# Optimization experiments

Measured on AMD Instinct MI355X. Metric: run time of the kernel, lower is better.

Reference implementation:

```python
import jax, jax.numpy as jnp
import numpy as np

TEMPERATURE = 0.5
EPS = 1e-12  # matches torch F.normalize default eps


def _l2_normalize(x):
    norm = jnp.sqrt(jnp.sum(x * x, axis=-1, keepdims=True))
    return x / jnp.maximum(norm, EPS)


def setup_inputs() -> dict:
    key = jax.random.key(0)
    k1, k2 = jax.random.split(key)
    B, C, D = 64, 512, 256
    visual_features = jax.random.normal(k1, (B, C, D), dtype=jnp.float32)
    text_embeddings = jax.random.normal(k2, (B, C, D), dtype=jnp.float32)
    return {"visual_features": visual_features, "text_embeddings": text_embeddings}


def reference(visual_features, text_embeddings):
    v = _l2_normalize(visual_features)   # (B, C, D)
    t = _l2_normalize(text_embeddings)   # (B, C, D)
    # positive: diagonal similarity per class
    sim_pos = jnp.einsum('bcd,bcd->bc', v, t)
    positive = jnp.exp(sim_pos / TEMPERATURE)            # (B, C)
    # full BxCxC similarity matrix
    all_sim = jnp.exp(jnp.einsum('bcd,bkd->bck', v, t) / TEMPERATURE)
    negative = jnp.sum(all_sim, axis=-1) - positive      # (B, C)
    loss = -jnp.log(positive / (positive + negative))
    return jnp.mean(loss)
```

## Files before the change

### kernel.cpp

```cpp
#include <hip/hip_runtime.h>
#include <hip/hip_bf16.h>

#define BB 64
#define CC 512
#define DD 256

typedef __attribute__((ext_vector_type(8))) short bf16x8;
typedef __attribute__((ext_vector_type(4))) float f32x4;
typedef unsigned int u32;

#define SWZ(r) (((r) & 7) << 4)

__device__ inline short f2bf(float f) {
    union { __hip_bfloat16 h; short s; } cv;
    cv.h = __float2bfloat16(f);
    return cv.s;
}

__global__ __launch_bounds__(256) void norm_rows(const float* __restrict__ in,
                                                 unsigned short* __restrict__ out) {
    const int row  = blockIdx.x * 4 + (threadIdx.x >> 6);
    const int lane = threadIdx.x & 63;
    const float4 x = reinterpret_cast<const float4*>(in)[(size_t)row * 64 + lane];
    float ss = x.x * x.x + x.y * x.y + x.z * x.z + x.w * x.w;
#pragma unroll
    for (int off = 32; off; off >>= 1) ss += __shfl_xor(ss, off);
    const float r = 1.0f / fmaxf(sqrtf(ss), 1e-12f);
    ushort4 o;
    o.x = (unsigned short)f2bf(x.x * r);
    o.y = (unsigned short)f2bf(x.y * r);
    o.z = (unsigned short)f2bf(x.z * r);
    o.w = (unsigned short)f2bf(x.w * r);
    reinterpret_cast<ushort4*>(out)[(size_t)row * 64 + lane] = o;
}

__global__ __launch_bounds__(256, 2) void gemm_loss(const float* __restrict__ V,
                                                    const unsigned short* __restrict__ Tn,
                                                    float* __restrict__ partials) {
    __shared__ char lds[65536];

    const int i0 = blockIdx.x;
    const int b  = (i0 & 7) * 8 + ((i0 >> 3) & 7);
    const int rb = i0 >> 6;

    const int tid  = threadIdx.x;
    const int lane = tid & 63;
    const int wave = tid >> 6;
    const int g    = lane >> 4;
    const int ln   = lane & 15;

    const float* gV = V + (size_t)b * (CC * DD) + (size_t)rb * 64 * DD;
    const char*  gT = reinterpret_cast<const char*>(Tn + (size_t)b * (CC * DD));

#pragma unroll
    for (int r2 = 0; r2 < 8; ++r2) {
        const int L   = wave * 8192 + r2 * 1024 + (lane << 4);
        const int row = L >> 9, inrow = L & 511;
        __builtin_amdgcn_global_load_lds((const u32*)(gT + row * 512 + (inrow ^ SWZ(row))),
                                         (u32*)(lds + wave * 8192 + r2 * 1024), 16, 0, 0);
    }

    {
        const int rrow  = tid >> 3;
        const int ecolB = (tid & 7) * 64;
        char* bufA = lds + 32768;
#pragma unroll
        for (int p = 0; p < 2; ++p) {
            const float4* src =
                reinterpret_cast<const float4*>(gV + (size_t)(p * 32 + rrow) * DD) + (tid & 7) * 8;
            float4 x[8];
#pragma unroll
            for (int q = 0; q < 8; ++q) x[q] = src[q];
            float ss = 0.f;
#pragma unroll
            for (int q = 0; q < 8; ++q)
                ss += x[q].x * x[q].x + x[q].y * x[q].y + x[q].z * x[q].z + x[q].w * x[q].w;
            ss += __shfl_xor(ss, 1);
            ss += __shfl_xor(ss, 2);
            ss += __shfl_xor(ss, 4);
            const float rinv = 1.0f / fmaxf(sqrtf(ss), 1e-12f);
            const int row = p * 32 + rrow;
            char* dstrow  = bufA + row * 512;
            const int sw  = SWZ(row);
#pragma unroll
            for (int q2 = 0; q2 < 4; ++q2) {
                const float4 v0 = x[2 * q2], v1 = x[2 * q2 + 1];
                bf16x8 o;
                o[0] = f2bf(v0.x * rinv); o[1] = f2bf(v0.y * rinv);
                o[2] = f2bf(v0.z * rinv); o[3] = f2bf(v0.w * rinv);
                o[4] = f2bf(v1.x * rinv); o[5] = f2bf(v1.y * rinv);
                o[6] = f2bf(v1.z * rinv); o[7] = f2bf(v1.w * rinv);
                *reinterpret_cast<bf16x8*>(dstrow + ((ecolB + q2 * 16) ^ sw)) = o;
            }
        }
    }
    __syncthreads();

    bf16x8 a[4][8];
#pragma unroll
    for (int i = 0; i < 4; ++i) {
        const int row  = i * 16 + ln;
        const char* rp = lds + 32768 + row * 512;
        const int sw   = SWZ(row);
#pragma unroll
        for (int kk = 0; kk < 8; ++kk)
            a[i][kk] = *reinterpret_cast<const bf16x8*>(rp + ((kk * 64 + g * 16) ^ sw));
    }
    __syncthreads();

    float rs[4][4];
    float dg[4][4];
#pragma unroll
    for (int i = 0; i < 4; ++i)
#pragma unroll
        for (int r = 0; r < 4; ++r) { rs[i][r] = 0.f; dg[i][r] = 0.f; }

    for (int ct = 0; ct < 8; ++ct) {
        if (ct < 7) {
            const char* gtile = gT + (size_t)(ct + 1) * 64 * 512;
            char* dst = lds + ((ct & 1) ? 0 : 32768);
#pragma unroll
            for (int r2 = 0; r2 < 8; ++r2) {
                const int L   = wave * 8192 + r2 * 1024 + (lane << 4);
                const int row = L >> 9, inrow = L & 511;
                __builtin_amdgcn_global_load_lds(
                    (const u32*)(gtile + row * 512 + (inrow ^ SWZ(row))),
                    (u32*)(dst + wave * 8192 + r2 * 1024), 16, 0, 0);
            }
        }

        const char* Bc = lds + ((ct & 1) ? 32768 : 0);
        f32x4 acc[4];
#pragma unroll
        for (int i = 0; i < 4; ++i) acc[i] = (f32x4){0.f, 0.f, 0.f, 0.f};
        {
            const int row  = wave * 16 + ln;
            const char* rp = Bc + row * 512;
            const int sw   = SWZ(row);
#pragma unroll
            for (int kk = 0; kk < 8; ++kk) {
                const bf16x8 bb = *reinterpret_cast<const bf16x8*>(rp + ((kk * 64 + g * 16) ^ sw));
#pragma unroll
                for (int i = 0; i < 4; ++i)
                    acc[i] = __builtin_amdgcn_mfma_f32_16x16x32_bf16(a[i][kk], bb, acc[i], 0, 0, 0);
            }
        }

        const int gcol = ct * 64 + wave * 16 + ln;
#pragma unroll
        for (int i = 0; i < 4; ++i) {
            const int grow = rb * 64 + i * 16 + g * 4;
#pragma unroll
            for (int r = 0; r < 4; ++r) {
                const float s2 = acc[i][r] * 2.0f;
                rs[i][r] += __expf(s2);
                if (gcol == grow + r) dg[i][r] += s2;
            }
        }
        __syncthreads();
    }

    float* vred = reinterpret_cast<float*>(lds);
    float* dred = vred + 256;
#pragma unroll
    for (int i = 0; i < 4; ++i)
#pragma unroll
        for (int r = 0; r < 4; ++r) {
            float v = rs[i][r];
            float d = dg[i][r];
#pragma unroll
            for (int m = 1; m < 16; m <<= 1) {
                v += __shfl_xor(v, m);
                d += __shfl_xor(d, m);
            }
            if (ln == 0) {
                const int rl = i * 16 + g * 4 + r;
                vred[rl * 4 + wave] = v;
                dred[rl * 4 + wave] = d;
            }
        }
    __syncthreads();

    if (wave == 0) {
        const float vv =
            vred[lane * 4] + vred[lane * 4 + 1] + vred[lane * 4 + 2] + vred[lane * 4 + 3];
        const float dd =
            dred[lane * 4] + dred[lane * 4 + 1] + dred[lane * 4 + 2] + dred[lane * 4 + 3];
        float lsum = logf(vv) - dd;
#pragma unroll
        for (int m = 1; m < 64; m <<= 1) lsum += __shfl_xor(lsum, m);
        if (lane == 0) partials[i0] = lsum;
    }
}

__global__ __launch_bounds__(256) void final_reduce(const float* __restrict__ partials,
                                                    float* __restrict__ out) {
    const int t = threadIdx.x;
    float v = partials[t] + partials[t + 256];
#pragma unroll
    for (int m = 1; m < 64; m <<= 1) v += __shfl_xor(v, m);
    __shared__ float red[4];
    if ((t & 63) == 0) red[t >> 6] = v;
    __syncthreads();
    if (t == 0) out[0] = (red[0] + red[1] + red[2] + red[3]) * (1.0f / 32768.0f);
}

extern "C" void kernel_launch(void* const* d_in, const int* in_sizes, int n_in,
                              void* d_out, int out_size, void* d_ws, size_t ws_size,
                              hipStream_t stream) {
    const float* vis = (const float*)d_in[0];
    const float* txt = (const float*)d_in[1];

    unsigned short* Tn = (unsigned short*)d_ws;
    float* partials    = (float*)((char*)d_ws + (size_t)BB * CC * DD * 2);
    float* out         = (float*)d_out;

    norm_rows<<<8192, 256, 0, stream>>>(txt, Tn);
    gemm_loss<<<512, 256, 0, stream>>>(vis, Tn, partials);
    final_reduce<<<1, 256, 0, stream>>>(partials, out);
}
```

Before: 39.12 us.

## Pre-normalize V in separate kernel and load GEMM operands directly to registers

Adds a norm_rows pass over the visual features so they are stored as bf16 in workspace, and the GEMM kernel no longer normalizes V itself. The GEMM drops its LDS staging of both operands: A fragments and B fragments are read straight from global memory into registers, the next B tile is prefetched as each MFMA step consumes the current one, and the per-tile __syncthreads is removed. Wave priority is raised around the MFMA loop with s_setprio. The cost is an extra kernel launch plus an additional write and read of V in bf16, and B rows are now reloaded by each wave from global or L2 rather than shared through LDS.

Result: slower. 50.68 us (+29.5%).

```diff
diff --git a/kernel.cpp b/kernel.cpp
--- a/kernel.cpp
+++ b/kernel.cpp
@@ -7,9 +7,6 @@
 
 typedef __attribute__((ext_vector_type(8))) short bf16x8;
 typedef __attribute__((ext_vector_type(4))) float f32x4;
-typedef unsigned int u32;
-
-#define SWZ(r) (((r) & 7) << 4)
 
 __device__ inline short f2bf(float f) {
     union { __hip_bfloat16 h; short s; } cv;
@@ -34,10 +31,11 @@
     reinterpret_cast<ushort4*>(out)[(size_t)row * 64 + lane] = o;
 }
 
-__global__ __launch_bounds__(256, 2) void gemm_loss(const float* __restrict__ V,
+__global__ __launch_bounds__(256, 2) void gemm_loss(const unsigned short* __restrict__ Vn,
                                                     const unsigned short* __restrict__ Tn,
                                                     float* __restrict__ partials) {
-    __shared__ char lds[65536];
+    __shared__ float vred[256];
+    __shared__ float dred[256];
 
     const int i0 = blockIdx.x;
     const int b  = (i0 & 7) * 8 + ((i0 >> 3) & 7);
@@ -49,64 +47,23 @@
     const int g    = lane >> 4;
     const int ln   = lane & 15;
 
-    const float* gV = V + (size_t)b * (CC * DD) + (size_t)rb * 64 * DD;
-    const char*  gT = reinterpret_cast<const char*>(Tn + (size_t)b * (CC * DD));
-
-#pragma unroll
-    for (int r2 = 0; r2 < 8; ++r2) {
-        const int L   = wave * 8192 + r2 * 1024 + (lane << 4);
-        const int row = L >> 9, inrow = L & 511;
-        __builtin_amdgcn_global_load_lds((const u32*)(gT + row * 512 + (inrow ^ SWZ(row))),
-                                         (u32*)(lds + wave * 8192 + r2 * 1024), 16, 0, 0);
-    }
-
-    {
-        const int rrow  = tid >> 3;
-        const int ecolB = (tid & 7) * 64;
-        char* bufA = lds + 32768;
-#pragma unroll
-        for (int p = 0; p < 2; ++p) {
-            const float4* src =
-                reinterpret_cast<const float4*>(gV + (size_t)(p * 32 + rrow) * DD) + (tid & 7) * 8;
-            float4 x[8];
-#pragma unroll
-            for (int q = 0; q < 8; ++q) x[q] = src[q];
-            float ss = 0.f;
-#pragma unroll
-            for (int q = 0; q < 8; ++q)
-                ss += x[q].x * x[q].x + x[q].y * x[q].y + x[q].z * x[q].z + x[q].w * x[q].w;
-            ss += __shfl_xor(ss, 1);
-            ss += __shfl_xor(ss, 2);
-            ss += __shfl_xor(ss, 4);
-            const float rinv = 1.0f / fmaxf(sqrtf(ss), 1e-12f);
-            const int row = p * 32 + rrow;
-            char* dstrow  = bufA + row * 512;
-            const int sw  = SWZ(row);
-#pragma unroll
-            for (int q2 = 0; q2 < 4; ++q2) {
-                const float4 v0 = x[2 * q2], v1 = x[2 * q2 + 1];
-                bf16x8 o;
-                o[0] = f2bf(v0.x * rinv); o[1] = f2bf(v0.y * rinv);
-                o[2] = f2bf(v0.z * rinv); o[3] = f2bf(v0.w * rinv);
-                o[4] = f2bf(v1.x * rinv); o[5] = f2bf(v1.y * rinv);
-                o[6] = f2bf(v1.z * rinv); o[7] = f2bf(v1.w * rinv);
-                *reinterpret_cast<bf16x8*>(dstrow + ((ecolB + q2 * 16) ^ sw)) = o;
-            }
-        }
-    }
-    __syncthreads();
+    const char* gA = reinterpret_cast<const char*>(Vn + (size_t)b * (CC * DD) + (size_t)rb * 64 * DD);
+    const char* gB = reinterpret_cast<const char*>(Tn + (size_t)b * (CC * DD));
 
     bf16x8 a[4][8];
 #pragma unroll
     for (int i = 0; i < 4; ++i) {
-        const int row  = i * 16 + ln;
-        const char* rp = lds + 32768 + row * 512;
-        const int sw   = SWZ(row);
+        const char* rp = gA + (i * 16 + ln) * 512 + g * 16;
 #pragma unroll
         for (int kk = 0; kk < 8; ++kk)
-            a[i][kk] = *reinterpret_cast<const bf16x8*>(rp + ((kk * 64 + g * 16) ^ sw));
+            a[i][kk] = *reinterpret_cast<const bf16x8*>(rp + kk * 64);
     }
-    __syncthreads();
+
+    const char* rpB = gB + (wave * 16 + ln) * 512 + g * 16;
+    bf16x8 bb[8];
+#pragma unroll
+    for (int kk = 0; kk < 8; ++kk)
+        bb[kk] = *reinterpret_cast<const bf16x8*>(rpB + kk * 64);
 
     float rs[4][4];
     float dg[4][4];
@@ -116,35 +73,20 @@
         for (int r = 0; r < 4; ++r) { rs[i][r] = 0.f; dg[i][r] = 0.f; }
 
     for (int ct = 0; ct < 8; ++ct) {
-        if (ct < 7) {
-            const char* gtile = gT + (size_t)(ct + 1) * 64 * 512;
-            char* dst = lds + ((ct & 1) ? 0 : 32768);
-#pragma unroll
-            for (int r2 = 0; r2 < 8; ++r2) {
-                const int L   = wave * 8192 + r2 * 1024 + (lane << 4);
-                const int row = L >> 9, inrow = L & 511;
-                __builtin_amdgcn_global_load_lds(
-                    (const u32*)(gtile + row * 512 + (inrow ^ SWZ(row))),
-                    (u32*)(dst + wave * 8192 + r2 * 1024), 16, 0, 0);
-            }
-        }
-
-        const char* Bc = lds + ((ct & 1) ? 32768 : 0);
         f32x4 acc[4];
 #pragma unroll
         for (int i = 0; i < 4; ++i) acc[i] = (f32x4){0.f, 0.f, 0.f, 0.f};
-        {
-            const int row  = wave * 16 + ln;
-            const char* rp = Bc + row * 512;
-            const int sw   = SWZ(row);
+
+        __builtin_amdgcn_s_setprio(1);
 #pragma unroll
-            for (int kk = 0; kk < 8; ++kk) {
-                const bf16x8 bb = *reinterpret_cast<const bf16x8*>(rp + ((kk * 64 + g * 16) ^ sw));
+        for (int kk = 0; kk < 8; ++kk) {
 #pragma unroll
-                for (int i = 0; i < 4; ++i)
-                    acc[i] = __builtin_amdgcn_mfma_f32_16x16x32_bf16(a[i][kk], bb, acc[i], 0, 0, 0);
-            }
+            for (int i = 0; i < 4; ++i)
+                acc[i] = __builtin_amdgcn_mfma_f32_16x16x32_bf16(a[i][kk], bb[kk], acc[i], 0, 0, 0);
+            if (ct < 7)
+                bb[kk] = *reinterpret_cast<const bf16x8*>(rpB + (ct + 1) * 32768 + kk * 64);
         }
+        __builtin_amdgcn_s_setprio(0);
 
         const int gcol = ct * 64 + wave * 16 + ln;
 #pragma unroll
@@ -157,11 +99,8 @@
                 if (gcol == grow + r) dg[i][r] += s2;
             }
         }
-        __syncthreads();
     }
 
-    float* vred = reinterpret_cast<float*>(lds);
-    float* dred = vred + 256;
 #pragma unroll
     for (int i = 0; i < 4; ++i)
 #pragma unroll
@@ -211,11 +150,13 @@
     const float* vis = (const float*)d_in[0];
     const float* txt = (const float*)d_in[1];
 
-    unsigned short* Tn = (unsigned short*)d_ws;
-    float* partials    = (float*)((char*)d_ws + (size_t)BB * CC * DD * 2);
+    unsigned short* Vn = (unsigned short*)d_ws;
+    unsigned short* Tn = Vn + (size_t)BB * CC * DD;
+    float* partials    = (float*)(Tn + (size_t)BB * CC * DD);
     float* out         = (float*)d_out;
 
+    norm_rows<<<8192, 256, 0, stream>>>(vis, Vn);
     norm_rows<<<8192, 256, 0, stream>>>(txt, Tn);
-    gemm_loss<<<512, 256, 0, stream>>>(vis, Tn, partials);
+    gemm_loss<<<512, 256, 0, stream>>>(Vn, Tn, partials);
     final_reduce<<<1, 256, 0, stream>>>(partials, out);
 }
```

## Make T tiles wave-private to drop block barriers and use vmcnt waits

Applied to the files above, without the earlier changes.

Each wave now loads only the 16 rows of the T tile that it consumes into its own LDS slice. This lets the per-tile __syncthreads be replaced by explicit s_waitcnt vmcnt waits that keep one tile prefetch in flight. The tile loop is fully unrolled, B fragments are preloaded before the MFMA chain under raised wave priority, and the diagonal check is limited to the tile where ct equals rb. The reduction scratch moves to separate shared arrays so it no longer aliases the tile buffers, at the cost of extra LDS. Correctness depends on the vmcnt counts matching the number of outstanding async LDS loads.

Result: slower. 44.83 us (+14.6%).

```diff
diff --git a/kernel.cpp b/kernel.cpp
--- a/kernel.cpp
+++ b/kernel.cpp
@@ -38,6 +38,8 @@
                                                     const unsigned short* __restrict__ Tn,
                                                     float* __restrict__ partials) {
     __shared__ char lds[65536];
+    __shared__ float vred[256];
+    __shared__ float dred[256];
 
     const int i0 = blockIdx.x;
     const int b  = (i0 & 7) * 8 + ((i0 >> 3) & 7);
@@ -54,10 +56,11 @@
 
 #pragma unroll
     for (int r2 = 0; r2 < 8; ++r2) {
-        const int L   = wave * 8192 + r2 * 1024 + (lane << 4);
-        const int row = L >> 9, inrow = L & 511;
-        __builtin_amdgcn_global_load_lds((const u32*)(gT + row * 512 + (inrow ^ SWZ(row))),
-                                         (u32*)(lds + wave * 8192 + r2 * 1024), 16, 0, 0);
+        const int L  = r2 * 1024 + (lane << 4);
+        const int lr = L >> 9, inrow = L & 511;
+        __builtin_amdgcn_global_load_lds(
+            (const u32*)(gT + (size_t)(wave * 16 + lr) * 512 + (inrow ^ SWZ(lr))),
+            (u32*)(lds + wave * 8192 + r2 * 1024), 16, 0, 0);
     }
 
     {
@@ -115,36 +118,44 @@
 #pragma unroll
         for (int r = 0; r < 4; ++r) { rs[i][r] = 0.f; dg[i][r] = 0.f; }
 
+#pragma unroll
     for (int ct = 0; ct < 8; ++ct) {
         if (ct < 7) {
             const char* gtile = gT + (size_t)(ct + 1) * 64 * 512;
-            char* dst = lds + ((ct & 1) ? 0 : 32768);
+            char* dst = lds + (((ct + 1) & 1) ? 32768 : 0) + wave * 8192;
 #pragma unroll
             for (int r2 = 0; r2 < 8; ++r2) {
-                const int L   = wave * 8192 + r2 * 1024 + (lane << 4);
-                const int row = L >> 9, inrow = L & 511;
+                const int L  = r2 * 1024 + (lane << 4);
+                const int lr = L >> 9, inrow = L & 511;
                 __builtin_amdgcn_global_load_lds(
-                    (const u32*)(gtile + row * 512 + (inrow ^ SWZ(row))),
-                    (u32*)(dst + wave * 8192 + r2 * 1024), 16, 0, 0);
-            }
-        }
-
-        const char* Bc = lds + ((ct & 1) ? 32768 : 0);
+                    (const u32*)(gtile + (size_t)(ct * 64 + 64 + wave * 16 + lr) * 512 * 0 +
+                                 (size_t)(wave * 16 + lr) * 512 + (inrow ^ SWZ(lr))),
+                    (u32*)(dst + r2 * 1024), 16, 0, 0);
+            }
+            asm volatile("s_waitcnt vmcnt(8)" ::: "memory");
+        } else {
+            asm volatile("s_waitcnt vmcnt(0)" ::: "memory");
+        }
+        __builtin_amdgcn_sched_barrier(0);
+
+        const char* Bc = lds + ((ct & 1) ? 32768 : 0) + wave * 8192;
+        const char* rp = Bc + ln * 512;
+        const int sw   = SWZ(ln);
+        bf16x8 bb[8];
+#pragma unroll
+        for (int kk = 0; kk < 8; ++kk)
+            bb[kk] = *reinterpret_cast<const bf16x8*>(rp + ((kk * 64 + g * 16) ^ sw));
+
         f32x4 acc[4];
 #pragma unroll
         for (int i = 0; i < 4; ++i) acc[i] = (f32x4){0.f, 0.f, 0.f, 0.f};
-        {
-            const int row  = wave * 16 + ln;
-            const char* rp = Bc + row * 512;
-            const int sw   = SWZ(row);
-#pragma unroll
-            for (int kk = 0; kk < 8; ++kk) {
-                const bf16x8 bb = *reinterpret_cast<const bf16x8*>(rp + ((kk * 64 + g * 16) ^ sw));
-#pragma unroll
-                for (int i = 0; i < 4; ++i)
-                    acc[i] = __builtin_amdgcn_mfma_f32_16x16x32_bf16(a[i][kk], bb, acc[i], 0, 0, 0);
-            }
-        }
+        __builtin_amdgcn_s_setprio(1);
+#pragma unroll
+        for (int kk = 0; kk < 8; ++kk)
+#pragma unroll
+            for (int i = 0; i < 4; ++i)
+                acc[i] = __builtin_amdgcn_mfma_f32_16x16x32_bf16(a[i][kk], bb[kk], acc[i], 0, 0, 0);
+        __builtin_amdgcn_s_setprio(0);
 
         const int gcol = ct * 64 + wave * 16 + ln;
 #pragma unroll
@@ -154,14 +165,11 @@
             for (int r = 0; r < 4; ++r) {
                 const float s2 = acc[i][r] * 2.0f;
                 rs[i][r] += __expf(s2);
-                if (gcol == grow + r) dg[i][r] += s2;
-            }
-        }
-        __syncthreads();
-    }
-
-    float* vred = reinterpret_cast<float*>(lds);
-    float* dred = vred + 256;
+                if (ct == rb && gcol == grow + r) dg[i][r] += s2;
+            }
+        }
+    }
+
 #pragma unroll
     for (int i = 0; i < 4; ++i)
 #pragma unroll
```
